# Kernel tuning notes

Hardware: AMD Instinct MI355X
Metric: run time of the kernel (lower is better)

The kernel has to match this reference:

```python
import jax, jax.numpy as jnp
import numpy as np

B, S, D, H = 2, 2048, 1024, 16
HD = D // H
NEG = -1000000000.0


def setup_inputs() -> dict:
    key = jax.random.key(0)
    k1, k2, k3, k4, k5, k6, k7 = jax.random.split(key, 7)
    scale = 1.0 / np.sqrt(D)
    return {
        "q": jax.random.normal(k1, (B, S, D), jnp.float32),
        "k": jax.random.normal(k2, (B, S, D), jnp.float32),
        "v": jax.random.normal(k3, (B, S, D), jnp.float32),
        # causal mask, broadcastable over (B, H, S, S)
        "mask": jnp.tril(jnp.ones((S, S), jnp.bool_))[None, None, :, :],
        "Wq": jax.random.normal(k4, (D, D), jnp.float32) * scale,
        "Wk": jax.random.normal(k5, (D, D), jnp.float32) * scale,
        "Wv": jax.random.normal(k6, (D, D), jnp.float32) * scale,
        "Wo": jax.random.normal(k7, (D, D), jnp.float32) * scale,
    }


def reference(q, k, v, mask, Wq, Wk, Wv, Wo):
    # nn.Linear(bias=False): y = x @ W.T
    qp = jnp.einsum("bsd,ed->bse", q, Wq).reshape(B, S, H, HD).transpose(0, 2, 1, 3)
    kp = jnp.einsum("bsd,ed->bse", k, Wk).reshape(B, S, H, HD).transpose(0, 2, 1, 3)
    vp = jnp.einsum("bsd,ed->bse", v, Wv).reshape(B, S, H, HD).transpose(0, 2, 1, 3)
    # scaled dot-product attention with masked softmax (dropout p=0)
    scores = jnp.einsum("bhqd,bhkd->bhqk", qp, kp) / jnp.sqrt(jnp.float32(HD))
    scores = jnp.where(mask, scores, NEG)
    attn = jax.nn.softmax(scores, axis=-1)
    ctx = jnp.einsum("bhqk,bhkd->bhqd", attn, vp)
    ctx = ctx.transpose(0, 2, 1, 3).reshape(B, S, D)
    return jnp.einsum("bsd,ed->bse", ctx, Wo)
```

## Files before the change

### kernel.cpp

```cpp
#include <hip/hip_runtime.h>

typedef __bf16 bf16;
typedef __bf16 bf16x4 __attribute__((ext_vector_type(4)));
typedef __bf16 bf16x8 __attribute__((ext_vector_type(8)));
typedef float f32x4 __attribute__((ext_vector_type(4)));
typedef float f32x16 __attribute__((ext_vector_type(16)));
typedef unsigned u32x4 __attribute__((ext_vector_type(4)));

static constexpr int Bn = 2, Sn = 2048, Dn = 1024, Hn = 16, HDn = 64;

__device__ __forceinline__ void gload_lds16(const void* g, void* l) {
  __builtin_amdgcn_global_load_lds((__attribute__((address_space(1))) void*)g,
                                   (__attribute__((address_space(3))) void*)l, 16, 0, 0);
}

__device__ __forceinline__ f32x4 mfma_bf16_16x16x32(bf16x8 a, bf16x8 b, f32x4 c) {
  return __builtin_amdgcn_mfma_f32_16x16x32_bf16(a, b, c, 0, 0, 0);
}

__device__ __forceinline__ f32x16 mfma_bf16_32x32x16(bf16x8 a, bf16x8 b, f32x16 c) {
  return __builtin_amdgcn_mfma_f32_32x32x16_bf16(a, b, c, 0, 0, 0);
}

__device__ __forceinline__ float fast_exp2(float x) {
  float r;
  asm("v_exp_f32 %0, %1" : "=v"(r) : "v"(x));
  return r;
}

__device__ __forceinline__ unsigned cvt_pk_bf16(float lo, float hi) {
  unsigned r;
  asm("v_cvt_pk_bf16_f32 %0, %1, %2" : "=v"(r) : "v"(lo), "v"(hi));
  return r;
}

__device__ __forceinline__ float cross_half_max(float v) {
  return fmaxf(v, __shfl_xor(v, 32, 64));
}
__device__ __forceinline__ float cross_half_add(float v) {
  return v + __shfl_xor(v, 32, 64);
}
__device__ __forceinline__ unsigned shfl32u(unsigned u) {
  return (unsigned)__shfl_xor((int)u, 32, 64);
}

#define WAITCNT_VM(N) asm volatile("s_waitcnt vmcnt(" #N ")" ::: "memory")
#define WAITCNT_LGKM0 asm volatile("s_waitcnt lgkmcnt(0)" ::: "memory")

struct CvtArgs {
  const float* in[7];
  bf16* out[7];
  int n4[7];
  float sc[7];
};

__global__ __launch_bounds__(256) void cvt_all(CvtArgs a) {
  const float* in = a.in[blockIdx.z];
  bf16* out = a.out[blockIdx.z];
  const int n4 = a.n4[blockIdx.z];
  const float s = a.sc[blockIdx.z];
  int i = blockIdx.x * 256 + threadIdx.x;
  const int stride = gridDim.x * 256;
  for (; i < n4; i += stride) {
    float4 v = reinterpret_cast<const float4*>(in)[i];
    bf16x4 o;
    o[0] = (bf16)(v.x * s); o[1] = (bf16)(v.y * s);
    o[2] = (bf16)(v.z * s); o[3] = (bf16)(v.w * s);
    reinterpret_cast<bf16x4*>(out)[i] = o;
  }
}

__device__ __forceinline__ void store_out(float* C, size_t i, float v) { C[i] = v; }
__device__ __forceinline__ void store_out(bf16* C, size_t i, float v) { C[i] = (bf16)v; }

template <typename OutT>
__device__ __forceinline__ void gemm_bt_dev(const bf16* __restrict__ A,
                                            const bf16* __restrict__ Bw,
                                            OutT* __restrict__ C,
                                            int K, int N, int row0, int col0) {
  const int t = threadIdx.x;
  const int l = t & 63, w = t >> 6;
  const int wr = w >> 1, wc = w & 1;
  const int lc = l & 15, lg = l >> 4;

  __shared__ bf16 As[128 * 32];
  __shared__ bf16 Bs[128 * 32];

  f32x4 acc[4][4] = {};

  for (int k0 = 0; k0 < K; k0 += 32) {
#pragma unroll
    for (int i = 0; i < 2; ++i) {
      const int c = i * 256 + t;
      const int r = c >> 2;
      const int scc = (c & 3) ^ (r & 3);
      gload_lds16(A + (size_t)(row0 + r) * K + k0 + scc * 8, As + c * 8);
      gload_lds16(Bw + (size_t)(col0 + r) * K + k0 + scc * 8, Bs + c * 8);
    }
    __syncthreads();

    bf16x8 af[4], bfr[4];
#pragma unroll
    for (int m = 0; m < 4; ++m) {
      const int r = wr * 64 + m * 16 + lc;
      af[m] = *reinterpret_cast<const bf16x8*>(As + r * 32 + ((lg ^ (r & 3)) * 8));
    }
#pragma unroll
    for (int n = 0; n < 4; ++n) {
      const int r = wc * 64 + n * 16 + lc;
      bfr[n] = *reinterpret_cast<const bf16x8*>(Bs + r * 32 + ((lg ^ (r & 3)) * 8));
    }
#pragma unroll
    for (int m = 0; m < 4; ++m)
#pragma unroll
      for (int n = 0; n < 4; ++n)
        acc[m][n] = mfma_bf16_16x16x32(af[m], bfr[n], acc[m][n]);
    __syncthreads();
  }

#pragma unroll
  for (int m = 0; m < 4; ++m) {
    const int rbase = row0 + wr * 64 + m * 16 + lg * 4;
#pragma unroll
    for (int n = 0; n < 4; ++n) {
      const int col = col0 + wc * 64 + n * 16 + lc;
#pragma unroll
      for (int j = 0; j < 4; ++j)
        store_out(C, (size_t)(rbase + j) * N + col, acc[m][n][j]);
    }
  }
}

__global__ __launch_bounds__(256) void gemm_qkv(
    const bf16* __restrict__ qa, const bf16* __restrict__ wq, bf16* __restrict__ qo,
    const bf16* __restrict__ ka, const bf16* __restrict__ wk, bf16* __restrict__ ko,
    const bf16* __restrict__ va, const bf16* __restrict__ wv, bf16* __restrict__ vo) {
  const int n = blockIdx.x;
  const int orig = (n & 7) * 96 + (n >> 3);
  const int x = orig & 7, y = (orig >> 3) & 31, z = orig >> 8;
  const bf16 *A, *Bw;
  bf16* C;
  if (z == 0)      { A = qa; Bw = wq; C = qo; }
  else if (z == 1) { A = ka; Bw = wk; C = ko; }
  else             { A = va; Bw = wv; C = vo; }
  gemm_bt_dev<bf16>(A, Bw, C, Dn, Dn, y * 128, x * 128);
}

__global__ __launch_bounds__(512) void gemm_out_f32(const bf16* __restrict__ A,
                                                    const bf16* __restrict__ Bw,
                                                    float* __restrict__ C) {
  const int n = blockIdx.x;
  const int orig = (n & 7) * 32 + (n >> 3);
  const int x = orig & 7, y = orig >> 3;
  const int row0 = y * 128, col0 = x * 128;

  const int t = threadIdx.x;
  const int half = t >> 8;
  const int tl = t & 255;
  const int l = tl & 63, wl = tl >> 6;
  const int wr = wl >> 1, wc = wl & 1;
  const int lc = l & 15, lg = l >> 4;

  __shared__ char smem[65536];
  bf16* As = (bf16*)(smem + half * 16384);
  bf16* Bs = (bf16*)(smem + half * 16384 + 8192);

  f32x4 acc[4][4] = {};
  const int kbase = half * 512;

  for (int k0i = 0; k0i < 512; k0i += 32) {
    const int k0 = kbase + k0i;
#pragma unroll
    for (int i = 0; i < 2; ++i) {
      const int c = i * 256 + tl;
      const int r = c >> 2;
      const int scc = (c & 3) ^ (r & 3);
      gload_lds16(A + (size_t)(row0 + r) * Dn + k0 + scc * 8, As + c * 8);
      gload_lds16(Bw + (size_t)(col0 + r) * Dn + k0 + scc * 8, Bs + c * 8);
    }
    __syncthreads();

    bf16x8 af[4], bfr[4];
#pragma unroll
    for (int m = 0; m < 4; ++m) {
      const int r = wr * 64 + m * 16 + lc;
      af[m] = *reinterpret_cast<const bf16x8*>(As + r * 32 + ((lg ^ (r & 3)) * 8));
    }
#pragma unroll
    for (int nn = 0; nn < 4; ++nn) {
      const int r = wc * 64 + nn * 16 + lc;
      bfr[nn] = *reinterpret_cast<const bf16x8*>(Bs + r * 32 + ((lg ^ (r & 3)) * 8));
    }
#pragma unroll
    for (int m = 0; m < 4; ++m)
#pragma unroll
      for (int nn = 0; nn < 4; ++nn)
        acc[m][nn] = mfma_bf16_16x16x32(af[m], bfr[nn], acc[m][nn]);
    __syncthreads();
  }

  float* Op = (float*)smem;
  if (half == 1) {
#pragma unroll
    for (int m = 0; m < 4; ++m) {
      const int rl = wr * 64 + m * 16 + lg * 4;
#pragma unroll
      for (int nn = 0; nn < 4; ++nn) {
        const int cl = wc * 64 + nn * 16 + lc;
#pragma unroll
        for (int j = 0; j < 4; ++j)
          Op[(rl + j) * 128 + cl] = acc[m][nn][j];
      }
    }
  }
  __syncthreads();

  if (half == 0) {
#pragma unroll
    for (int m = 0; m < 4; ++m) {
      const int rl = wr * 64 + m * 16 + lg * 4;
#pragma unroll
      for (int nn = 0; nn < 4; ++nn) {
        const int cl = wc * 64 + nn * 16 + lc;
#pragma unroll
        for (int j = 0; j < 4; ++j)
          C[(size_t)(row0 + rl + j) * Dn + col0 + cl] =
              acc[m][nn][j] + Op[(rl + j) * 128 + cl];
      }
    }
  }
}

__global__ __launch_bounds__(256) void transpose_bsd(const bf16* __restrict__ in,
                                                     bf16* __restrict__ out) {
  __shared__ bf16 tile[64][66];
  const int s0 = blockIdx.x * 64, d0 = blockIdx.y * 64, b = blockIdx.z;
  const int t = threadIdx.x;
#pragma unroll
  for (int i = 0; i < 2; ++i) {
    const int c = i * 256 + t;
    const int r = c >> 3, cc = (c & 7) * 8;
    const bf16x8 v = *reinterpret_cast<const bf16x8*>(
        in + ((size_t)b * Sn + s0 + r) * Dn + d0 + cc);
#pragma unroll
    for (int j = 0; j < 8; ++j) tile[r][cc + j] = v[j];
  }
  __syncthreads();
#pragma unroll
  for (int i = 0; i < 2; ++i) {
    const int c = i * 256 + t;
    const int r = c >> 3, cc = (c & 7) * 8;
    bf16x8 v;
#pragma unroll
    for (int j = 0; j < 8; ++j) v[j] = tile[cc + j][r];
    *reinterpret_cast<bf16x8*>(out + ((size_t)b * Dn + d0 + r) * Sn + s0 + cc) = v;
  }
}

__global__ __launch_bounds__(512) void flash_attn(const bf16* __restrict__ qp,
                                                  const bf16* __restrict__ kp,
                                                  const bf16* __restrict__ vt,
                                                  bf16* __restrict__ ctx) {
  const int n = blockIdx.x;
  const int g = (n & 7) + 8 * (n >> 6);
  const int pid = (n >> 3) & 7;
  const int h = g & 15;
  const int b = g >> 4;
  const int t = threadIdx.x, w = t >> 6, l = t & 63;
  const int lq = l & 31, hi = l >> 5;
  const int half = w >> 2;

  __shared__ char smem[81920];
  char* my = smem + half * 40960;

  const int tl = t & 255;
  const int rl = tl >> 3;
  const int scc = (tl & 7) ^ (rl & 7);
  const bf16* kbase = kp + ((size_t)b * Sn + rl) * Dn + h * HDn + scc * 8;
  const bf16* vbase = vt + ((size_t)b * Dn + h * HDn + rl) * Sn + scc * 8;

  for (int ph = 0; ph < 2; ++ph) {
    const int qt = ph ? pid : 15 - pid;
    const int qrow0 = qt * 128 + (w & 3) * 32;
    const int cnt = qt + 1;
    const int tbase = half * cnt;

    auto STAGE = [&](int i) {
      const int kv0 = (tbase + i) * 64;
      char* Kd = my + (i & 1) * 8192 + tl * 16;
      char* Vd = my + 16384 + (i % 3) * 8192 + tl * 16;
      const bf16* ks = kbase + (size_t)kv0 * Dn;
      const bf16* vs = vbase + kv0;
#pragma unroll
      for (int ii = 0; ii < 2; ++ii) {
        gload_lds16(ks + (size_t)ii * 32 * Dn, Kd + ii * 4096);
        gload_lds16(vs + (size_t)ii * 32 * Sn, Vd + ii * 4096);
      }
    };

    bf16x8 qf[4];
#pragma unroll
    for (int kk = 0; kk < 4; ++kk)
      qf[kk] = *reinterpret_cast<const bf16x8*>(
          qp + ((size_t)b * Sn + qrow0 + lq) * Dn + h * HDn + kk * 16 + hi * 8);

    f32x16 oacc0 = {}, oacc1 = {};
    float mrow = -1e30f, lsum = 0.0f;

    auto QK = [&](int i, f32x16& s0_, f32x16& s1_) {
      const char* Kc = my + (i & 1) * 8192;
      __builtin_amdgcn_s_setprio(1);
#pragma unroll
      for (int kk = 0; kk < 4; ++kk) {
        const int ch = kk * 2 + hi;
        const int r0 = lq, r1 = 32 + lq;
        const bf16x8 k0 = *reinterpret_cast<const bf16x8*>(Kc + r0 * 128 + ((ch ^ (r0 & 7)) << 4));
        const bf16x8 k1 = *reinterpret_cast<const bf16x8*>(Kc + r1 * 128 + ((ch ^ (r1 & 7)) << 4));
        s0_ = mfma_bf16_32x32x16(k0, qf[kk], s0_);
        s1_ = mfma_bf16_32x32x16(k1, qf[kk], s1_);
      }
      __builtin_amdgcn_s_setprio(0);
    };

    auto SMPV = [&](int i, f32x16& s0, f32x16& s1) {
      const int kv0 = (tbase + i) * 64;
      const char* Vc = my + 16384 + (i % 3) * 8192;

      if (kv0 + 63 > qrow0) {
        const int qg = qrow0 + lq;
#pragma unroll
        for (int r = 0; r < 16; ++r) {
          const int kvl = (r & 3) + 8 * (r >> 2) + 4 * hi;
          if (kv0 + kvl > qg)      s0[r] = -1e30f;
          if (kv0 + 32 + kvl > qg) s1[r] = -1e30f;
        }
      }

      float mx[8];
#pragma unroll
      for (int i2 = 0; i2 < 8; ++i2)
        mx[i2] = fmaxf(fmaxf(s0[i2], s0[i2 + 8]), fmaxf(s1[i2], s1[i2 + 8]));
#pragma unroll
      for (int i2 = 0; i2 < 4; ++i2) mx[i2] = fmaxf(mx[i2], mx[i2 + 4]);
      const float tmax_own = fmaxf(fmaxf(mx[0], mx[1]), fmaxf(mx[2], mx[3]));
      const float tmax = cross_half_max(tmax_own);

      float alpha = 1.0f;
      if (!__all(tmax <= mrow + 8.0f)) {
        const float mn = fmaxf(mrow, tmax);
        alpha = fast_exp2(mrow - mn);
        mrow = mn;
#pragma unroll
        for (int r = 0; r < 16; ++r) { oacc0[r] *= alpha; oacc1[r] *= alpha; }
      }
#pragma unroll
      for (int r = 0; r < 16; ++r) {
        s0[r] = fast_exp2(s0[r] - mrow);
        s1[r] = fast_exp2(s1[r] - mrow);
      }
      float sm[8];
#pragma unroll
      for (int i2 = 0; i2 < 8; ++i2)
        sm[i2] = (s0[i2] + s0[i2 + 8]) + (s1[i2] + s1[i2 + 8]);
#pragma unroll
      for (int i2 = 0; i2 < 4; ++i2) sm[i2] += sm[i2 + 4];
      float rsum = (sm[0] + sm[1]) + (sm[2] + sm[3]);
      rsum = cross_half_add(rsum);
      lsum = lsum * alpha + rsum;

      u32x4 pw[4];
#pragma unroll
      for (int c2 = 0; c2 < 4; ++c2) {
        const f32x16& S = (c2 < 2) ? s0 : s1;
        const int base = (c2 & 1) * 8;
        const unsigned u0 = cvt_pk_bf16(S[base + 0], S[base + 1]);
        const unsigned u1 = cvt_pk_bf16(S[base + 2], S[base + 3]);
        const unsigned u2 = cvt_pk_bf16(S[base + 4], S[base + 5]);
        const unsigned u3 = cvt_pk_bf16(S[base + 6], S[base + 7]);
        const unsigned r1 = shfl32u(hi ? u0 : u2);
        const unsigned r2 = shfl32u(hi ? u1 : u3);
        pw[c2][0] = hi ? r1 : u0;
        pw[c2][1] = hi ? r2 : u1;
        pw[c2][2] = hi ? u2 : r1;
        pw[c2][3] = hi ? u3 : r2;
      }

      __builtin_amdgcn_s_setprio(1);
#pragma unroll
      for (int kk = 0; kk < 4; ++kk) {
        const bf16x8 pf = __builtin_bit_cast(bf16x8, pw[kk]);
        const int ch = kk * 2 + hi;
        const int r0 = lq, r1 = 32 + lq;
        const bf16x8 v0 = *reinterpret_cast<const bf16x8*>(Vc + r0 * 128 + ((ch ^ (r0 & 7)) << 4));
        const bf16x8 v1 = *reinterpret_cast<const bf16x8*>(Vc + r1 * 128 + ((ch ^ (r1 & 7)) << 4));
        oacc0 = mfma_bf16_32x32x16(v0, pf, oacc0);
        oacc1 = mfma_bf16_32x32x16(v1, pf, oacc1);
      }
      __builtin_amdgcn_s_setprio(0);
    };

    __builtin_amdgcn_s_barrier();
    __builtin_amdgcn_sched_barrier(0);

    STAGE(0);
    if (cnt > 1) { STAGE(1); WAITCNT_VM(4); } else { WAITCNT_VM(0); }
    __builtin_amdgcn_sched_barrier(0);
    __builtin_amdgcn_s_barrier();
    __builtin_amdgcn_sched_barrier(0);

    f32x16 sp0 = {}, sp1 = {};
    if (tbase * 64 <= qrow0 + 31) QK(0, sp0, sp1);

    for (int i = 0; i < cnt; ++i) {
      WAITCNT_VM(0);
      __builtin_amdgcn_sched_barrier(0);
      __builtin_amdgcn_s_barrier();
      __builtin_amdgcn_sched_barrier(0);

      if (i + 2 < cnt) STAGE(i + 2);
      f32x16 sn0 = {}, sn1 = {};
      if (i + 1 < cnt && (tbase + i + 1) * 64 <= qrow0 + 31) QK(i + 1, sn0, sn1);
      if ((tbase + i) * 64 <= qrow0 + 31) SMPV(i, sp0, sp1);
      sp0 = sn0; sp1 = sn1;
      WAITCNT_LGKM0;
    }

    __builtin_amdgcn_s_barrier();
    __builtin_amdgcn_sched_barrier(0);

    float* Op = (float*)smem;
    float* Ml = (float*)(smem + 33280);
    const int lrow = (w & 3) * 32 + lq;

    if (half == 1) {
#pragma unroll
      for (int r = 0; r < 16; ++r) {
        const int d = (r & 3) + 8 * (r >> 2) + 4 * hi;
        Op[lrow * 65 + d]      = oacc0[r];
        Op[lrow * 65 + 32 + d] = oacc1[r];
      }
      if (hi == 0) { Ml[lrow] = mrow; Ml[128 + lrow] = lsum; }
    }
    WAITCNT_LGKM0;
    __builtin_amdgcn_s_barrier();
    __builtin_amdgcn_sched_barrier(0);

    if (half == 0) {
      const float m1 = Ml[lrow], l1 = Ml[128 + lrow];
      const float mm = fmaxf(mrow, m1);
      const float a0 = fast_exp2(mrow - mm);
      const float a1 = fast_exp2(m1 - mm);
      const float inv = 1.0f / (lsum * a0 + l1 * a1);

      bf16* ep = (bf16*)(smem + 40960 + w * 4608);
#pragma unroll
      for (int dt = 0; dt < 2; ++dt) {
        const f32x16& O = dt ? oacc1 : oacc0;
#pragma unroll
        for (int g2 = 0; g2 < 4; ++g2) {
          bf16x4 o4;
#pragma unroll
          for (int jj = 0; jj < 4; ++jj) {
            const int d = dt * 32 + 8 * g2 + 4 * hi + jj;
            const float o1 = Op[lrow * 65 + d];
            o4[jj] = (bf16)((O[g2 * 4 + jj] * a0 + o1 * a1) * inv);
          }
          const int d0 = dt * 32 + g2 * 8 + hi * 4;
          *reinterpret_cast<bf16x4*>(&ep[lq * 72 + d0]) = o4;
        }
      }
      WAITCNT_LGKM0;
      __builtin_amdgcn_sched_barrier(0);
#pragma unroll
      for (int i = 0; i < 4; ++i) {
        const int q = i * 8 + (l >> 3);
        const int d0 = (l & 7) * 8;
        const bf16x8 vv = *reinterpret_cast<const bf16x8*>(&ep[q * 72 + d0]);
        *reinterpret_cast<bf16x8*>(
            &ctx[((size_t)b * Sn + qrow0 + q) * Dn + h * HDn + d0]) = vv;
      }
    }
  }
}

extern "C" void kernel_launch(void* const* d_in, const int* in_sizes, int n_in,
                              void* d_out, int out_size, void* d_ws, size_t ws_size,
                              hipStream_t stream) {
  const float* q  = (const float*)d_in[0];
  const float* k  = (const float*)d_in[1];
  const float* v  = (const float*)d_in[2];
  const float* Wq = (const float*)d_in[4];
  const float* Wk = (const float*)d_in[5];
  const float* Wv = (const float*)d_in[6];
  const float* Wo = (const float*)d_in[7];

  constexpr size_t BSD = (size_t)Bn * Sn * Dn;
  constexpr size_t DD  = (size_t)Dn * Dn;

  char* p = (char*)d_ws;
  bf16* qbf = (bf16*)p; p += BSD * 2;
  bf16* kbf = (bf16*)p; p += BSD * 2;
  bf16* vbf = (bf16*)p; p += BSD * 2;
  bf16* qpb = (bf16*)p; p += BSD * 2;
  bf16* kpb = (bf16*)p; p += BSD * 2;
  bf16* vpb = (bf16*)p; p += BSD * 2;
  bf16* wqb = (bf16*)p; p += DD * 2;
  bf16* wkb = (bf16*)p; p += DD * 2;
  bf16* wvb = (bf16*)p; p += DD * 2;
  bf16* wob = (bf16*)p; p += DD * 2;
  bf16* vtb  = kbf;
  bf16* ctxb = qbf;

  const float wq_scale = 0.125f * 1.4426950408889634f;

  CvtArgs ca;
  ca.in[0] = q;  ca.out[0] = qbf; ca.n4[0] = (int)(BSD / 4); ca.sc[0] = 1.0f;
  ca.in[1] = k;  ca.out[1] = kbf; ca.n4[1] = (int)(BSD / 4); ca.sc[1] = 1.0f;
  ca.in[2] = v;  ca.out[2] = vbf; ca.n4[2] = (int)(BSD / 4); ca.sc[2] = 1.0f;
  ca.in[3] = Wq; ca.out[3] = wqb; ca.n4[3] = (int)(DD / 4);  ca.sc[3] = wq_scale;
  ca.in[4] = Wk; ca.out[4] = wkb; ca.n4[4] = (int)(DD / 4);  ca.sc[4] = 1.0f;
  ca.in[5] = Wv; ca.out[5] = wvb; ca.n4[5] = (int)(DD / 4);  ca.sc[5] = 1.0f;
  ca.in[6] = Wo; ca.out[6] = wob; ca.n4[6] = (int)(DD / 4);  ca.sc[6] = 1.0f;
  cvt_all<<<dim3(1024, 1, 7), 256, 0, stream>>>(ca);

  gemm_qkv<<<dim3(768), 256, 0, stream>>>(
      qbf, wqb, qpb, kbf, wkb, kpb, vbf, wvb, vpb);

  transpose_bsd<<<dim3(Sn / 64, Dn / 64, Bn), 256, 0, stream>>>(vpb, vtb);

  flash_attn<<<dim3(256), 512, 0, stream>>>(qpb, kpb, vtb, ctxb);

  gemm_out_f32<<<dim3(256), 512, 0, stream>>>(ctxb, wob, (float*)d_out);

  (void)in_sizes; (void)n_in; (void)out_size; (void)ws_size;
}
```

Before: 116.8 us.

## Fuse fp32-to-bf16 activation conversion into QKV projection GEMM

The separate conversion pass over q, k and v is removed. The QKV GEMM now loads fp32 activation tiles directly into LDS, with a swizzle, and converts them to bf16 in registers before the MFMA. Only the weights are still converted in a smaller pre-pass. This avoids writing and re-reading three bf16 activation tensors, at the cost of twice the LDS traffic for the A tile and extra conversion work inside the GEMM loop.

Result: faster. 108.8 us (-6.9%).

```diff
diff --git a/kernel.cpp b/kernel.cpp
--- a/kernel.cpp
+++ b/kernel.cpp
@@ -48,20 +48,19 @@
 #define WAITCNT_LGKM0 asm volatile("s_waitcnt lgkmcnt(0)" ::: "memory")
 
 struct CvtArgs {
-  const float* in[7];
-  bf16* out[7];
-  int n4[7];
-  float sc[7];
+  const float* in[4];
+  bf16* out[4];
+  int n4;
+  float sc[4];
 };
 
-__global__ __launch_bounds__(256) void cvt_all(CvtArgs a) {
+__global__ __launch_bounds__(256) void cvt_w4(CvtArgs a) {
   const float* in = a.in[blockIdx.z];
   bf16* out = a.out[blockIdx.z];
-  const int n4 = a.n4[blockIdx.z];
   const float s = a.sc[blockIdx.z];
   int i = blockIdx.x * 256 + threadIdx.x;
   const int stride = gridDim.x * 256;
-  for (; i < n4; i += stride) {
+  for (; i < a.n4; i += stride) {
     float4 v = reinterpret_cast<const float4*>(in)[i];
     bf16x4 o;
     o[0] = (bf16)(v.x * s); o[1] = (bf16)(v.y * s);
@@ -132,18 +131,84 @@
 }
 
 __global__ __launch_bounds__(256) void gemm_qkv(
-    const bf16* __restrict__ qa, const bf16* __restrict__ wq, bf16* __restrict__ qo,
-    const bf16* __restrict__ ka, const bf16* __restrict__ wk, bf16* __restrict__ ko,
-    const bf16* __restrict__ va, const bf16* __restrict__ wv, bf16* __restrict__ vo) {
+    const float* __restrict__ qa, const bf16* __restrict__ wq, bf16* __restrict__ qo,
+    const float* __restrict__ ka, const bf16* __restrict__ wk, bf16* __restrict__ ko,
+    const float* __restrict__ va, const bf16* __restrict__ wv, bf16* __restrict__ vo) {
   const int n = blockIdx.x;
   const int orig = (n & 7) * 96 + (n >> 3);
   const int x = orig & 7, y = (orig >> 3) & 31, z = orig >> 8;
-  const bf16 *A, *Bw;
-  bf16* C;
+  const float* A; const bf16* Bw; bf16* C;
   if (z == 0)      { A = qa; Bw = wq; C = qo; }
   else if (z == 1) { A = ka; Bw = wk; C = ko; }
   else             { A = va; Bw = wv; C = vo; }
-  gemm_bt_dev<bf16>(A, Bw, C, Dn, Dn, y * 128, x * 128);
+
+  const int t = threadIdx.x;
+  const int l = t & 63, w = t >> 6;
+  const int wr = w >> 1, wc = w & 1;
+  const int lc = l & 15, lg = l >> 4;
+  const int row0 = y * 128, col0 = x * 128;
+
+  __shared__ float Asf[128 * 32];
+  __shared__ bf16  Bs[128 * 32];
+
+  f32x4 acc[4][4] = {};
+
+  for (int k0 = 0; k0 < Dn; k0 += 32) {
+#pragma unroll
+    for (int i = 0; i < 4; ++i) {
+      const int c = i * 256 + t;
+      const int r = c >> 3;
+      const int sj = (c & 7) ^ (r & 7);
+      gload_lds16(A + (size_t)(row0 + r) * Dn + k0 + sj * 4, (char*)Asf + c * 16);
+    }
+#pragma unroll
+    for (int i = 0; i < 2; ++i) {
+      const int c = i * 256 + t;
+      const int r = c >> 2;
+      const int scc = (c & 3) ^ (r & 3);
+      gload_lds16(Bw + (size_t)(col0 + r) * Dn + k0 + scc * 8, Bs + c * 8);
+    }
+    __syncthreads();
+
+    bf16x8 af[4], bfr[4];
+#pragma unroll
+    for (int m = 0; m < 4; ++m) {
+      const int r = wr * 64 + m * 16 + lc;
+      const int sA = (2 * lg) ^ (r & 7);
+      const int sB2 = (2 * lg + 1) ^ (r & 7);
+      const float4 fa = *reinterpret_cast<const float4*>(Asf + r * 32 + sA * 4);
+      const float4 fb = *reinterpret_cast<const float4*>(Asf + r * 32 + sB2 * 4);
+      u32x4 u;
+      u[0] = cvt_pk_bf16(fa.x, fa.y);
+      u[1] = cvt_pk_bf16(fa.z, fa.w);
+      u[2] = cvt_pk_bf16(fb.x, fb.y);
+      u[3] = cvt_pk_bf16(fb.z, fb.w);
+      af[m] = __builtin_bit_cast(bf16x8, u);
+    }
+#pragma unroll
+    for (int nn = 0; nn < 4; ++nn) {
+      const int r = wc * 64 + nn * 16 + lc;
+      bfr[nn] = *reinterpret_cast<const bf16x8*>(Bs + r * 32 + ((lg ^ (r & 3)) * 8));
+    }
+#pragma unroll
+    for (int m = 0; m < 4; ++m)
+#pragma unroll
+      for (int nn = 0; nn < 4; ++nn)
+        acc[m][nn] = mfma_bf16_16x16x32(af[m], bfr[nn], acc[m][nn]);
+    __syncthreads();
+  }
+
+#pragma unroll
+  for (int m = 0; m < 4; ++m) {
+    const int rbase = row0 + wr * 64 + m * 16 + lg * 4;
+#pragma unroll
+    for (int nn = 0; nn < 4; ++nn) {
+      const int col = col0 + wc * 64 + nn * 16 + lc;
+#pragma unroll
+      for (int j = 0; j < 4; ++j)
+        C[(size_t)(rbase + j) * Dn + col + 0] = (bf16)acc[m][nn][j];
+    }
+  }
 }
 
 __global__ __launch_bounds__(512) void gemm_out_f32(const bf16* __restrict__ A,
@@ -498,9 +563,9 @@
   constexpr size_t DD  = (size_t)Dn * Dn;
 
   char* p = (char*)d_ws;
-  bf16* qbf = (bf16*)p; p += BSD * 2;
-  bf16* kbf = (bf16*)p; p += BSD * 2;
-  bf16* vbf = (bf16*)p; p += BSD * 2;
+  bf16* ctxb = (bf16*)p; p += BSD * 2;
+  bf16* vtb  = (bf16*)p; p += BSD * 2;
+  p += BSD * 2;
   bf16* qpb = (bf16*)p; p += BSD * 2;
   bf16* kpb = (bf16*)p; p += BSD * 2;
   bf16* vpb = (bf16*)p; p += BSD * 2;
@@ -508,23 +573,19 @@
   bf16* wkb = (bf16*)p; p += DD * 2;
   bf16* wvb = (bf16*)p; p += DD * 2;
   bf16* wob = (bf16*)p; p += DD * 2;
-  bf16* vtb  = kbf;
-  bf16* ctxb = qbf;
 
   const float wq_scale = 0.125f * 1.4426950408889634f;
 
   CvtArgs ca;
-  ca.in[0] = q;  ca.out[0] = qbf; ca.n4[0] = (int)(BSD / 4); ca.sc[0] = 1.0f;
-  ca.in[1] = k;  ca.out[1] = kbf; ca.n4[1] = (int)(BSD / 4); ca.sc[1] = 1.0f;
-  ca.in[2] = v;  ca.out[2] = vbf; ca.n4[2] = (int)(BSD / 4); ca.sc[2] = 1.0f;
-  ca.in[3] = Wq; ca.out[3] = wqb; ca.n4[3] = (int)(DD / 4);  ca.sc[3] = wq_scale;
-  ca.in[4] = Wk; ca.out[4] = wkb; ca.n4[4] = (int)(DD / 4);  ca.sc[4] = 1.0f;
-  ca.in[5] = Wv; ca.out[5] = wvb; ca.n4[5] = (int)(DD / 4);  ca.sc[5] = 1.0f;
-  ca.in[6] = Wo; ca.out[6] = wob; ca.n4[6] = (int)(DD / 4);  ca.sc[6] = 1.0f;
-  cvt_all<<<dim3(1024, 1, 7), 256, 0, stream>>>(ca);
+  ca.in[0] = Wq; ca.out[0] = wqb; ca.sc[0] = wq_scale;
+  ca.in[1] = Wk; ca.out[1] = wkb; ca.sc[1] = 1.0f;
+  ca.in[2] = Wv; ca.out[2] = wvb; ca.sc[2] = 1.0f;
+  ca.in[3] = Wo; ca.out[3] = wob; ca.sc[3] = 1.0f;
+  ca.n4 = (int)(DD / 4);
+  cvt_w4<<<dim3(256, 1, 4), 256, 0, stream>>>(ca);
 
   gemm_qkv<<<dim3(768), 256, 0, stream>>>(
-      qbf, wqb, qpb, kbf, wkb, kpb, vbf, wvb, vpb);
+      q, wqb, qpb, k, wkb, kpb, v, wvb, vpb);
 
   transpose_bsd<<<dim3(Sn / 64, Dn / 64, Bn), 256, 0, stream>>>(vpb, vtb);
 
```
